# Performance work log

Measured on AMD Instinct MI355X. Metric: run time of the kernel, lower is better.

Reference implementation:

```python
import jax, jax.numpy as jnp
import numpy as np

B, S = 2, 1024
IN, OUT = 1024, 1024
N_IN, N_OUT = 32, 32          # isqrt(IN), isqrt(OUT)
CD = 64                       # compressed_feature_dim
K = 2                         # num_monarchs
D1 = N_IN * N_IN * N_OUT      # 32768, flat M1 size per token
D2 = N_OUT * N_IN * N_OUT     # 32768, flat M2 size per token


def setup_inputs() -> dict:
    key = jax.random.key(0)
    ks = jax.random.split(key, 13)
    g = lambda k, shape, s=0.02: jax.random.normal(k, shape, dtype=jnp.float32) * s
    return {
        "x":  jax.random.normal(ks[0], (B, S, IN), dtype=jnp.float32),
        "Wc": g(ks[1], (IN, CD)),  "bc": g(ks[2], (CD,)),
        "W1": g(ks[3], (K, CD, D1)), "b1": g(ks[4], (K, D1)),
        "W2": g(ks[5], (K, CD, D2)), "b2": g(ks[6], (K, D2)),
        "Wm": g(ks[7], (CD, K)),   "bm": g(ks[8], (K,)),
        "Wb": g(ks[9], (CD, OUT)), "bb": g(ks[10], (OUT,)),
        "Wr": g(ks[11], (CD, 1)),  "br": g(ks[12], (1,)),
    }


def reference(x, Wc, bc, W1, b1, W2, b2, Wm, bm, Wb, bb, Wr, br):
    b, s, _ = x.shape
    # compressor: Linear + Tanh -> [B,S,CD]
    cf = jnp.tanh(x @ Wc + bc)
    # per-expert generated flat weights: [B,S,K,D]
    gen1 = jnp.einsum('bsc,kcd->bskd', cf, W1) + b1
    gen2 = jnp.einsum('bsc,kcd->bskd', cf, W2) + b2
    # expert mixing coefficients -> softmax over K
    coeffs = jax.nn.softmax(cf @ Wm + bm, axis=-1)  # [B,S,K]
    M1f = jnp.einsum('bskd,bsk->bsd', gen1, coeffs)
    M2f = jnp.einsum('bskd,bsk->bsd', gen2, coeffs)
    # Monarch block matmul with per-token weights
    M1 = M1f.reshape(b, s, N_IN, N_IN, N_OUT)   # g=N_IN blocks of [N_IN,N_OUT]
    M2 = M2f.reshape(b, s, N_OUT, N_IN, N_OUT)  # g=N_OUT blocks of [N_IN,N_OUT]
    x1 = x.reshape(b, s, N_IN, N_IN)
    h1 = jnp.einsum('bsgi,bsgio->bsgo', x1, M1)      # [B,S,N_IN,N_OUT]
    h1t = jnp.swapaxes(h1, -1, -2)                   # [B,S,N_OUT,N_IN]
    h2 = jnp.einsum('bsgi,bsgio->bsgo', h1t, M2)     # [B,S,N_OUT,N_OUT]
    y = h2.reshape(b, s, OUT)
    # per-token scale and bias
    ratio = cf @ Wr + br                             # [B,S,1]
    bias = cf @ Wb + bb                              # [B,S,OUT]
    return y * ratio + bias
```

## Files before the change

kernel.cpp:

```cpp
#include <hip/hip_runtime.h>
#include <cstddef>

typedef unsigned short ushortT;
typedef short s8v __attribute__((ext_vector_type(8)));
typedef float f32x4 __attribute__((ext_vector_type(4)));

constexpr int NTOK = 2048;

__device__ inline ushortT f2bf(float f) {
  unsigned u = __float_as_uint(f);
  u += 0x7fffu + ((u >> 16) & 1u);
  return (ushortT)(u >> 16);
}

__device__ inline void gl_lds16(const s8v* g, s8v* l) {
  __builtin_amdgcn_global_load_lds(
      (const __attribute__((address_space(1))) unsigned int*)g,
      (__attribute__((address_space(3))) unsigned int*)l, 16, 0, 0);
}

__global__ __launch_bounds__(256) void setup_kernel(
    const float* __restrict__ x, const float* __restrict__ Wc, const float* __restrict__ bc,
    const float* __restrict__ Wm, const float* __restrict__ bm,
    const float* __restrict__ Wr, const float* __restrict__ br,
    const float* __restrict__ W1, const float* __restrict__ b1,
    const float* __restrict__ W2, const float* __restrict__ b2,
    const float* __restrict__ Wb, const float* __restrict__ bb,
    ushortT* __restrict__ FP, float* __restrict__ ratio,
    ushortT* __restrict__ P1, ushortT* __restrict__ P2, ushortT* __restrict__ WbP)
{
  __shared__ __align__(16) char smem[16384];
  const int tid = threadIdx.x;
  const int bid = blockIdx.x;

  if (bid < 256) {
    float* part = (float*)smem;
    float* cf_s = part + 2048;
    float* a0s  = cf_s + 512;
    float* a1s  = a0s + 8;
    const int c = tid & 63;
    const int q = tid >> 6;
    const int t0 = bid * 8;

    float acc[8];
#pragma unroll
    for (int p = 0; p < 8; ++p) acc[p] = 0.f;
    const float* xq = x + (size_t)t0 * 1024 + q * 256;
    const float* wq = Wc + (size_t)(q * 256) * 64 + c;
#pragma unroll 4
    for (int jj = 0; jj < 64; ++jj) {
      float w0 = wq[(jj * 4 + 0) * 64];
      float w1 = wq[(jj * 4 + 1) * 64];
      float w2 = wq[(jj * 4 + 2) * 64];
      float w3 = wq[(jj * 4 + 3) * 64];
#pragma unroll
      for (int p = 0; p < 8; ++p) {
        float4 xv = *(const float4*)(xq + (size_t)p * 1024 + jj * 4);
        acc[p] = fmaf(xv.x, w0, acc[p]);
        acc[p] = fmaf(xv.y, w1, acc[p]);
        acc[p] = fmaf(xv.z, w2, acc[p]);
        acc[p] = fmaf(xv.w, w3, acc[p]);
      }
    }
#pragma unroll
    for (int p = 0; p < 8; ++p) part[(q * 8 + p) * 64 + c] = acc[p];
    __syncthreads();

#pragma unroll
    for (int r = 0; r < 2; ++r) {
      int idx = tid + r * 256;
      int p = idx >> 6, cc = idx & 63;
      float s = part[(0 * 8 + p) * 64 + cc] + part[(1 * 8 + p) * 64 + cc] +
                part[(2 * 8 + p) * 64 + cc] + part[(3 * 8 + p) * 64 + cc] + bc[cc];
      cf_s[p * 64 + cc] = tanhf(s);
    }
    __syncthreads();

#pragma unroll 1
    for (int pp = 0; pp < 2; ++pp) {
      int p = q * 2 + pp;
      float cf = cf_s[p * 64 + c];
      float z0 = cf * Wm[2 * c], z1 = cf * Wm[2 * c + 1], rr = cf * Wr[c];
      for (int off = 32; off; off >>= 1) {
        z0 += __shfl_down(z0, off);
        z1 += __shfl_down(z1, off);
        rr += __shfl_down(rr, off);
      }
      if (c == 0) {
        z0 += bm[0]; z1 += bm[1];
        float mx = fmaxf(z0, z1);
        float e0 = expf(z0 - mx), e1 = expf(z1 - mx);
        float a0 = e0 / (e0 + e1);
        a0s[p] = a0;
        a1s[p] = 1.0f - a0;
        ratio[t0 + p] = rr + br[0];
      }
    }
    __syncthreads();

    const int ks0 = c >> 5, kk = c & 31;
    const int slot = (kk >> 3) * 16, e = kk & 7;
#pragma unroll
    for (int pp = 0; pp < 2; ++pp) {
      int p = q * 2 + pp;
      int t = t0 + p, tt = t >> 4, tok = t & 15;
      size_t base = (size_t)tt * 2560;
      float cf = cf_s[p * 64 + c];
      float a0 = a0s[p], a1 = a1s[p];
      FP[base + (size_t)ks0 * 512 + (slot + tok) * 8 + e]       = f2bf(a0 * cf);
      FP[base + (size_t)(2 + ks0) * 512 + (slot + tok) * 8 + e] = f2bf(a1 * cf);
      if (c < 32) {
        float v = (c == 0) ? a0 : (c == 1) ? a1 : 0.0f;
        FP[base + 4 * 512 + ((c >> 3) * 16 + tok) * 8 + (c & 7)] = f2bf(v);
      }
    }
  } else {
    ushortT (*lds)[1024] = (ushortT (*)[1024])smem;
    int pb = bid - 256;
    int fac, g, jc8;
    if (pb < 1280) { fac = pb / 640; int rem = pb % 640; g = rem / 20; jc8 = rem % 20; }
    else           { fac = 2; g = 0; jc8 = pb - 1280; }
    const float* W  = (fac == 0) ? W1 : W2;
    const float* bv = (fac == 0) ? b1 : b2;
    ushortT* P = (fac == 0) ? P1 : (fac == 1) ? P2 : WbP;
    const int c4 = tid;

#pragma unroll
    for (int rl = 0; rl < 8; ++rl) {
      int jj = jc8 * 8 + rl;
      float4 v = make_float4(0.f, 0.f, 0.f, 0.f);
      if (fac < 2) {
        if (jj < 128)       v = *(const float4*)(W  + (size_t)jj * 32768 + g * 1024 + c4 * 4);
        else if (jj < 130)  v = *(const float4*)(bv + (size_t)(jj - 128) * 32768 + g * 1024 + c4 * 4);
      } else {
        if (jj < 128)       v = *(const float4*)(Wb + (size_t)(jj & 63) * 1024 + c4 * 4);
        else if (jj < 130)  v = *(const float4*)(bb + c4 * 4);
      }
      int col0 = c4 * 4;
      int sw = col0 ^ ((col0 >> 4) & 0x1C);
      ushortT* d = &lds[rl][sw];
      d[0] = f2bf(v.x); d[1] = f2bf(v.y); d[2] = f2bf(v.z); d[3] = f2bf(v.w);
    }
    __syncthreads();
    const int ks = jc8 >> 2, kkg = jc8 & 3;
#pragma unroll
    for (int it = 0; it < 4; ++it) {
      int idx = tid + it * 256;
      int ct_l = idx >> 4, cl = idx & 15;
      int scol;
      if (fac < 2) {
        int o = ct_l >> 1, ib = (ct_l & 1) * 16;
        scol = (ib + cl) * 32 + o;
      } else {
        scol = ct_l * 16 + cl;
      }
      scol ^= ((scol >> 4) & 0x1C);
      ushortT v[8];
#pragma unroll
      for (int e = 0; e < 8; ++e) v[e] = lds[e][scol];
      size_t ctile = (fac < 2) ? (size_t)(g * 64 + ct_l) : (size_t)ct_l;
      size_t off = ctile * 2560 + (size_t)ks * 512 + (kkg * 16 + cl) * 8;
      uint4 qv;
      qv.x = v[0] | ((unsigned)v[1] << 16);
      qv.y = v[2] | ((unsigned)v[3] << 16);
      qv.z = v[4] | ((unsigned)v[5] << 16);
      qv.w = v[6] | ((unsigned)v[7] << 16);
      *(uint4*)(P + off) = qv;
    }
  }
}

template <int PASS>
__global__ __launch_bounds__(256, 2) void mm_kernel(
    const s8v* __restrict__ fP, const s8v* __restrict__ wP,
    const s8v* __restrict__ wbP,
    const float* __restrict__ xg,
    const float* __restrict__ rat,
    float* __restrict__ outp)
{
  __shared__ s8v bsh[2][1280];
  __shared__ float xsf[(PASS == 1 ? 2 : 1) * 2112];
  __shared__ float hs[PASS == 2 ? 64 : 1][9];
  __shared__ float bls[PASS == 2 ? 64 : 1][9];
  const int tid = threadIdx.x;
  const int lane = tid & 63;
  const int w = tid >> 6;
  const int bid = blockIdx.x;
  const int cb  = (bid & 7) * 16 + (bid >> 6);
  const int tbg = (bid >> 3) & 7;
  const int g = cb >> 2;

  const s8v* ap = wP + (size_t)(cb * 16 + w * 4) * 320 + lane;
  s8v a[4][5];
#pragma unroll
  for (int i = 0; i < 4; ++i)
#pragma unroll
    for (int ks = 0; ks < 5; ++ks) a[i][ks] = ap[i * 320 + ks * 64];

  s8v ab[5];
  if constexpr (PASS == 2) {
    const s8v* abp = wbP + (size_t)(cb >> 1) * 320 + lane;
#pragma unroll
    for (int ks = 0; ks < 5; ++ks) ab[ks] = abp[ks * 64];
  }

  const s8v* fbase = fP + (size_t)(tbg * 4) * 1280;

#pragma unroll
  for (int c2 = 0; c2 < 5; ++c2)
    gl_lds16(fbase + w * 320 + c2 * 64 + lane, &bsh[0][w * 320 + c2 * 64]);
  __syncthreads();

#pragma unroll 1
  for (int tt2 = 0; tt2 < 4; ++tt2) {
    const int buf = tt2 & 1;
    const int t0 = (tbg * 4 + tt2) * 64;

    float4 xv[2];
#pragma unroll
    for (int it = 0; it < 2; ++it) {
      int idx = tid + it * 256;
      if (PASS == 1) {
        int t = idx >> 3, i4 = idx & 7;
        xv[it] = *(const float4*)(xg + (size_t)(t0 + t) * 1024 + g * 32 + i4 * 4);
      } else {
        int i = idx >> 4, tq = idx & 15;
        xv[it] = *(const float4*)(xg + (size_t)(i * 32 + g) * 2048 + t0 + tq * 4);
      }
    }
    if (tt2 < 3) {
      const s8v* fn = fbase + (size_t)(tt2 + 1) * 1280;
#pragma unroll
      for (int c2 = 0; c2 < 5; ++c2)
        gl_lds16(fn + w * 320 + c2 * 64 + lane, &bsh[buf ^ 1][w * 320 + c2 * 64]);
    }

    f32x4 acc[4][4];
#pragma unroll
    for (int i = 0; i < 4; ++i)
#pragma unroll
      for (int j = 0; j < 4; ++j) acc[i][j] = {0.f, 0.f, 0.f, 0.f};
    f32x4 accb = {0.f, 0.f, 0.f, 0.f};

#pragma unroll
    for (int ks = 0; ks < 5; ++ks) {
      s8v b0 = bsh[buf][0 * 320 + ks * 64 + lane];
      s8v b1 = bsh[buf][1 * 320 + ks * 64 + lane];
      s8v b2 = bsh[buf][2 * 320 + ks * 64 + lane];
      s8v b3 = bsh[buf][3 * 320 + ks * 64 + lane];
      if constexpr (PASS == 2) {
        s8v bw = bsh[buf][w * 320 + ks * 64 + lane];
        accb = __builtin_amdgcn_mfma_f32_16x16x32_bf16(ab[ks], bw, accb, 0, 0, 0);
      }
#pragma unroll
      for (int i = 0; i < 4; ++i) {
        acc[i][0] = __builtin_amdgcn_mfma_f32_16x16x32_bf16(a[i][ks], b0, acc[i][0], 0, 0, 0);
        acc[i][1] = __builtin_amdgcn_mfma_f32_16x16x32_bf16(a[i][ks], b1, acc[i][1], 0, 0, 0);
        acc[i][2] = __builtin_amdgcn_mfma_f32_16x16x32_bf16(a[i][ks], b2, acc[i][2], 0, 0, 0);
        acc[i][3] = __builtin_amdgcn_mfma_f32_16x16x32_bf16(a[i][ks], b3, acc[i][3], 0, 0, 0);
      }
    }

#pragma unroll
    for (int it = 0; it < 2; ++it) {
      int idx = tid + it * 256;
      float* d;
      if (PASS == 1) { int t = idx >> 3, i4 = idx & 7; d = &xsf[buf * 2112 + t * 33 + i4 * 4]; }
      else           { int i = idx >> 4, tq = idx & 15; d = &xsf[i * 66 + tq * 4]; }
      d[0] = xv[it].x; d[1] = xv[it].y; d[2] = xv[it].z; d[3] = xv[it].w;
    }
    __syncthreads();

    const int tau = lane & 15, q = lane >> 4;
#pragma unroll
    for (int tt = 0; tt < 4; ++tt) {
      int tl = tt * 16 + tau;
#pragma unroll
      for (int run = 0; run < 2; ++run) {
        float sacc = 0.f;
#pragma unroll
        for (int ch = 0; ch < 2; ++ch) {
          int ct = run * 2 + ch;
          f32x4 av = acc[ct][tt];
#pragma unroll
          for (int r = 0; r < 4; ++r) {
            int i = ch * 16 + q * 4 + r;
            float xvv = (PASS == 1) ? xsf[buf * 2112 + tl * 33 + i] : xsf[i * 66 + tl];
            sacc = fmaf(av[r], xvv, sacc);
          }
        }
        sacc += __shfl_xor(sacc, 16);
        sacc += __shfl_xor(sacc, 32);
        if constexpr (PASS == 1) {
          if (lane < 16) {
            int colg = g * 32 + (cb & 3) * 8 + w * 2 + run;
            outp[(size_t)colg * 2048 + t0 + tt * 16 + tau] = sacc;
          }
        } else {
          if (lane < 16) hs[tl][w * 2 + run] = sacc;
        }
      }
    }
    if constexpr (PASS == 2) {
      if ((lane >> 5) == (cb & 1)) {
        int ol = ((lane >> 4) & 1) * 4;
#pragma unroll
        for (int r = 0; r < 4; ++r) bls[w * 16 + tau][ol + r] = accb[r];
      }
      __syncthreads();
      if (tid < 128) {
        int row = tid >> 1, half = tid & 1;
        int t = t0 + row;
        int col = g * 32 + (cb & 3) * 8 + half * 4;
        float r = rat[t];
        float4 o;
        o.x = fmaf(hs[row][half * 4 + 0], r, bls[row][half * 4 + 0]);
        o.y = fmaf(hs[row][half * 4 + 1], r, bls[row][half * 4 + 1]);
        o.z = fmaf(hs[row][half * 4 + 2], r, bls[row][half * 4 + 2]);
        o.w = fmaf(hs[row][half * 4 + 3], r, bls[row][half * 4 + 3]);
        *(float4*)(outp + (size_t)t * 1024 + col) = o;
      }
    }
  }
}

extern "C" void kernel_launch(void* const* d_in, const int* in_sizes, int n_in,
                              void* d_out, int out_size, void* d_ws, size_t ws_size,
                              hipStream_t stream) {
  const float* x  = (const float*)d_in[0];
  const float* Wc = (const float*)d_in[1];
  const float* bc = (const float*)d_in[2];
  const float* W1 = (const float*)d_in[3];
  const float* b1 = (const float*)d_in[4];
  const float* W2 = (const float*)d_in[5];
  const float* b2 = (const float*)d_in[6];
  const float* Wm = (const float*)d_in[7];
  const float* bm = (const float*)d_in[8];
  const float* Wb = (const float*)d_in[9];
  const float* bb = (const float*)d_in[10];
  const float* Wr = (const float*)d_in[11];
  const float* br = (const float*)d_in[12];
  float* out = (float*)d_out;

  ushortT* P1  = (ushortT*)d_ws;
  ushortT* P2  = P1 + (size_t)2048 * 2560;
  ushortT* WbP = P2 + (size_t)2048 * 2560;
  ushortT* FP  = WbP + (size_t)64 * 2560;
  float* ratio = (float*)(FP + (size_t)128 * 2560);
  float* h1T   = ratio + NTOK;

  setup_kernel<<<dim3(1556), dim3(256), 0, stream>>>(
      x, Wc, bc, Wm, bm, Wr, br, W1, b1, W2, b2, Wb, bb, FP, ratio, P1, P2, WbP);
  mm_kernel<1><<<dim3(1024), dim3(256), 0, stream>>>(
      (const s8v*)FP, (const s8v*)P1, (const s8v*)WbP, x, nullptr, h1T);
  mm_kernel<2><<<dim3(1024), dim3(256), 0, stream>>>(
      (const s8v*)FP, (const s8v*)P2, (const s8v*)WbP, h1T, ratio, out);
}
```

Baseline: 80.17 us.

## Rebalance work split: more setup blocks, fewer mm blocks with longer token loops

The setup kernel's compressor path now gives each block 4 tokens instead of 8, doubling its block count to spread the x@Wc work across more CUs. The matmul kernels launch half as many blocks, each looping over 8 token tiles instead of 4, so the per-block register-resident weight fragments are reused over more tokens. MFMA sections are wrapped in s_setprio to favor issue of the matrix instructions. Fewer mm blocks (512 on a 256-CU part) may reduce occupancy and lengthen each block's serial chain.

```diff
diff --git a/kernel.cpp b/kernel.cpp
--- a/kernel.cpp
+++ b/kernel.cpp
@@ -33,18 +33,18 @@
   const int tid = threadIdx.x;
   const int bid = blockIdx.x;
 
-  if (bid < 256) {
+  if (bid < 512) {
     float* part = (float*)smem;
-    float* cf_s = part + 2048;
-    float* a0s  = cf_s + 512;
-    float* a1s  = a0s + 8;
+    float* cf_s = part + 1024;
+    float* a0s  = cf_s + 256;
+    float* a1s  = a0s + 4;
     const int c = tid & 63;
     const int q = tid >> 6;
-    const int t0 = bid * 8;
-
-    float acc[8];
-#pragma unroll
-    for (int p = 0; p < 8; ++p) acc[p] = 0.f;
+    const int t0 = bid * 4;
+
+    float acc[4];
+#pragma unroll
+    for (int p = 0; p < 4; ++p) acc[p] = 0.f;
     const float* xq = x + (size_t)t0 * 1024 + q * 256;
     const float* wq = Wc + (size_t)(q * 256) * 64 + c;
 #pragma unroll 4
@@ -54,7 +54,7 @@
       float w2 = wq[(jj * 4 + 2) * 64];
       float w3 = wq[(jj * 4 + 3) * 64];
 #pragma unroll
-      for (int p = 0; p < 8; ++p) {
+      for (int p = 0; p < 4; ++p) {
         float4 xv = *(const float4*)(xq + (size_t)p * 1024 + jj * 4);
         acc[p] = fmaf(xv.x, w0, acc[p]);
         acc[p] = fmaf(xv.y, w1, acc[p]);
@@ -63,23 +63,19 @@
       }
     }
 #pragma unroll
-    for (int p = 0; p < 8; ++p) part[(q * 8 + p) * 64 + c] = acc[p];
-    __syncthreads();
-
-#pragma unroll
-    for (int r = 0; r < 2; ++r) {
-      int idx = tid + r * 256;
-      int p = idx >> 6, cc = idx & 63;
-      float s = part[(0 * 8 + p) * 64 + cc] + part[(1 * 8 + p) * 64 + cc] +
-                part[(2 * 8 + p) * 64 + cc] + part[(3 * 8 + p) * 64 + cc] + bc[cc];
+    for (int p = 0; p < 4; ++p) part[(q * 4 + p) * 64 + c] = acc[p];
+    __syncthreads();
+
+    {
+      int p = tid >> 6, cc = tid & 63;
+      float s = part[(0 + p) * 64 + cc] + part[(4 + p) * 64 + cc] +
+                part[(8 + p) * 64 + cc] + part[(12 + p) * 64 + cc] + bc[cc];
       cf_s[p * 64 + cc] = tanhf(s);
     }
     __syncthreads();
 
-#pragma unroll 1
-    for (int pp = 0; pp < 2; ++pp) {
-      int p = q * 2 + pp;
-      float cf = cf_s[p * 64 + c];
+    {
+      float cf = cf_s[q * 64 + c];
       float z0 = cf * Wm[2 * c], z1 = cf * Wm[2 * c + 1], rr = cf * Wr[c];
       for (int off = 32; off; off >>= 1) {
         z0 += __shfl_down(z0, off);
@@ -91,22 +87,20 @@
         float mx = fmaxf(z0, z1);
         float e0 = expf(z0 - mx), e1 = expf(z1 - mx);
         float a0 = e0 / (e0 + e1);
-        a0s[p] = a0;
-        a1s[p] = 1.0f - a0;
-        ratio[t0 + p] = rr + br[0];
+        a0s[q] = a0;
+        a1s[q] = 1.0f - a0;
+        ratio[t0 + q] = rr + br[0];
       }
     }
     __syncthreads();
 
     const int ks0 = c >> 5, kk = c & 31;
     const int slot = (kk >> 3) * 16, e = kk & 7;
-#pragma unroll
-    for (int pp = 0; pp < 2; ++pp) {
-      int p = q * 2 + pp;
-      int t = t0 + p, tt = t >> 4, tok = t & 15;
+    {
+      int t = t0 + q, tt = t >> 4, tok = t & 15;
       size_t base = (size_t)tt * 2560;
-      float cf = cf_s[p * 64 + c];
-      float a0 = a0s[p], a1 = a1s[p];
+      float cf = cf_s[q * 64 + c];
+      float a0 = a0s[q], a1 = a1s[q];
       FP[base + (size_t)ks0 * 512 + (slot + tok) * 8 + e]       = f2bf(a0 * cf);
       FP[base + (size_t)(2 + ks0) * 512 + (slot + tok) * 8 + e] = f2bf(a1 * cf);
       if (c < 32) {
@@ -116,7 +110,7 @@
     }
   } else {
     ushortT (*lds)[1024] = (ushortT (*)[1024])smem;
-    int pb = bid - 256;
+    int pb = bid - 512;
     int fac, g, jc8;
     if (pb < 1280) { fac = pb / 640; int rem = pb % 640; g = rem / 20; jc8 = rem % 20; }
     else           { fac = 2; g = 0; jc8 = pb - 1280; }
@@ -186,8 +180,8 @@
   const int lane = tid & 63;
   const int w = tid >> 6;
   const int bid = blockIdx.x;
-  const int cb  = (bid & 7) * 16 + (bid >> 6);
-  const int tbg = (bid >> 3) & 7;
+  const int cb  = (bid & 7) * 16 + (bid >> 5);
+  const int tbgh = (bid >> 3) & 3;
   const int g = cb >> 2;
 
   const s8v* ap = wP + (size_t)(cb * 16 + w * 4) * 320 + lane;
@@ -204,7 +198,7 @@
     for (int ks = 0; ks < 5; ++ks) ab[ks] = abp[ks * 64];
   }
 
-  const s8v* fbase = fP + (size_t)(tbg * 4) * 1280;
+  const s8v* fbase = fP + (size_t)(tbgh * 8) * 1280;
 
 #pragma unroll
   for (int c2 = 0; c2 < 5; ++c2)
@@ -212,9 +206,9 @@
   __syncthreads();
 
 #pragma unroll 1
-  for (int tt2 = 0; tt2 < 4; ++tt2) {
+  for (int tt2 = 0; tt2 < 8; ++tt2) {
     const int buf = tt2 & 1;
-    const int t0 = (tbg * 4 + tt2) * 64;
+    const int t0 = (tbgh * 8 + tt2) * 64;
 
     float4 xv[2];
 #pragma unroll
@@ -228,7 +222,7 @@
         xv[it] = *(const float4*)(xg + (size_t)(i * 32 + g) * 2048 + t0 + tq * 4);
       }
     }
-    if (tt2 < 3) {
+    if (tt2 < 7) {
       const s8v* fn = fbase + (size_t)(tt2 + 1) * 1280;
 #pragma unroll
       for (int c2 = 0; c2 < 5; ++c2)
@@ -242,6 +236,7 @@
       for (int j = 0; j < 4; ++j) acc[i][j] = {0.f, 0.f, 0.f, 0.f};
     f32x4 accb = {0.f, 0.f, 0.f, 0.f};
 
+    __builtin_amdgcn_s_setprio(1);
 #pragma unroll
     for (int ks = 0; ks < 5; ++ks) {
       s8v b0 = bsh[buf][0 * 320 + ks * 64 + lane];
@@ -260,6 +255,7 @@
         acc[i][3] = __builtin_amdgcn_mfma_f32_16x16x32_bf16(a[i][ks], b3, acc[i][3], 0, 0, 0);
       }
     }
+    __builtin_amdgcn_s_setprio(0);
 
 #pragma unroll
     for (int it = 0; it < 2; ++it) {
@@ -349,10 +345,10 @@
   float* ratio = (float*)(FP + (size_t)128 * 2560);
   float* h1T   = ratio + NTOK;
 
-  setup_kernel<<<dim3(1556), dim3(256), 0, stream>>>(
+  setup_kernel<<<dim3(1812), dim3(256), 0, stream>>>(
       x, Wc, bc, Wm, bm, Wr, br, W1, b1, W2, b2, Wb, bb, FP, ratio, P1, P2, WbP);
-  mm_kernel<1><<<dim3(1024), dim3(256), 0, stream>>>(
+  mm_kernel<1><<<dim3(512), dim3(256), 0, stream>>>(
       (const s8v*)FP, (const s8v*)P1, (const s8v*)WbP, x, nullptr, h1T);
-  mm_kernel<2><<<dim3(1024), dim3(256), 0, stream>>>(
+  mm_kernel<2><<<dim3(512), dim3(256), 0, stream>>>(
       (const s8v*)FP, (const s8v*)P2, (const s8v*)WbP, h1T, ratio, out);
 }
```

Result: faster. 77.13 us (median of 4 runs) (-3.8%).
